# Optimization experiments

Hardware: AMD Instinct MI355X
Metric: run time of the kernel (lower is better)

The kernel has to match this reference:

```python
import jax, jax.numpy as jnp
import numpy as np

EPS = 1e-5

def conv3d(x, w):
    # x: [B,C,D,H,W], w: [O,I,3,3,3], stride 1, padding 1 (size preserving)
    return jax.lax.conv_general_dilated(
        x, w, window_strides=(1, 1, 1),
        padding=((1, 1), (1, 1), (1, 1)),
        dimension_numbers=('NCDHW', 'OIDHW', 'NCDHW'))

def deconv3d(x, w):
    # ConvTranspose3d(k=3, s=1, p=1) == conv3d with spatially flipped kernel, in/out swapped
    # torch ConvTranspose3d weight layout: [in, out, kD, kH, kW]
    wc = jnp.flip(w, axis=(2, 3, 4)).transpose(1, 0, 2, 3, 4)
    return conv3d(x, wc)

def batchnorm(x, bn):
    # bn: [4, C] rows = (gamma, beta, running_mean, running_var); inference mode
    g, b, m, v = bn[0], bn[1], bn[2], bn[3]
    scale = g * jax.lax.rsqrt(v + EPS)
    shift = b - m * scale
    return x * scale[None, :, None, None, None] + shift[None, :, None, None, None]

def qrnn_scan(Z, F, reverse):
    # gated linear recurrence h_t = f_t*h_{t-1} + (1-f_t)*z_t over depth axis (dim 2)
    Zs = jnp.moveaxis(Z, 2, 0)  # [D,B,C,H,W]
    Fs = jnp.moveaxis(F, 2, 0)
    def step(h, zf):
        z, f = zf
        h = f * h + (1.0 - f) * z
        return h, h
    h0 = jnp.zeros_like(Zs[0])  # h=None in torch == h=0 since f*0 vanishes
    _, hs = jax.lax.scan(step, h0, (Zs, Fs), reverse=reverse)
    return jnp.moveaxis(hs, 0, 2)

def qrnn_layer(x, w, bn, hidden, reverse, upsample, transpose):
    if upsample:
        # nn.Upsample(scale_factor=(1,2,2)) nearest
        x = jnp.repeat(jnp.repeat(x, 2, axis=3), 2, axis=4)
    g = deconv3d(x, w) if transpose else conv3d(x, w)
    g = batchnorm(g, bn)
    Z, F = g[:, :hidden], g[:, hidden:]
    return qrnn_scan(jnp.tanh(Z), jax.nn.sigmoid(F), reverse)

def setup_inputs():
    key = jax.random.key(0)
    ks = jax.random.split(key, 12)
    B, D = 4, 31
    x = jax.random.normal(ks[0], (B, 64, D, 32, 32), jnp.float32)
    xs2 = jax.random.normal(ks[1], (B, 32, D, 64, 64), jnp.float32)
    xs1 = jax.random.normal(ks[2], (B, 32, D, 64, 64), jnp.float32)
    xs0 = jax.random.normal(ks[3], (B, 16, D, 128, 128), jnp.float32)
    def wconv(k, shape):
        fan_in = shape[1] * 27
        return jax.random.normal(k, shape, jnp.float32) / np.float32(np.sqrt(fan_in))
    # layer0: UpsampleConv3d 64 -> 32 hidden (gates 64): Conv3d weight [64,64,3,3,3]
    w0 = wconv(ks[4], (64, 64, 3, 3, 3))
    # layer1: DeConv3D 32 -> 32 hidden (gates 64): ConvTranspose weight [in=32,out=64,3,3,3]
    w1 = wconv(ks[5], (32, 64, 3, 3, 3))
    # layer2: UpsampleConv3d 32 -> 16 hidden (gates 32): Conv3d weight [32,32,3,3,3]
    w2 = wconv(ks[6], (32, 32, 3, 3, 3))
    # layer3: DeConv3D 16 -> 16 hidden (gates 32): ConvTranspose weight [16,32,3,3,3]
    w3 = wconv(ks[7], (16, 32, 3, 3, 3))
    def mkbn(k, c):
        k1, k2, k3, k4 = jax.random.split(k, 4)
        return jnp.stack([
            jax.random.uniform(k1, (c,), jnp.float32, 0.5, 1.5),   # gamma
            jax.random.normal(k2, (c,), jnp.float32) * 0.1,        # beta
            jax.random.normal(k3, (c,), jnp.float32) * 0.1,        # running mean
            jax.random.uniform(k4, (c,), jnp.float32, 0.5, 1.5)])  # running var
    bn0 = mkbn(ks[8], 64)
    bn1 = mkbn(ks[9], 64)
    bn2 = mkbn(ks[10], 32)
    bn3 = mkbn(ks[11], 32)
    return dict(x=x, xs0=xs0, xs1=xs1, xs2=xs2,
                w0=w0, w1=w1, w2=w2, w3=w3,
                bn0=bn0, bn1=bn1, bn2=bn2, bn3=bn3)

def reference(x, xs0, xs1, xs2, w0, w1, w2, w3, bn0, bn1, bn2, bn3):
    # QRNN3DDecoder.forward with has_ad=True, reverse=False; scan direction alternates.
    # xs are popped last-first: xs2, xs1, xs0.
    h = qrnn_layer(x, w0, bn0, 32, False, True, False)          # upsample conv -> [B,32,D,64,64]
    h = qrnn_layer(h + xs2, w1, bn1, 32, True, False, True)     # deconv        -> [B,32,D,64,64]
    h = qrnn_layer(h + xs1, w2, bn2, 16, False, True, False)    # upsample conv -> [B,16,D,128,128]
    h = qrnn_layer(h + xs0, w3, bn3, 16, True, False, True)     # deconv        -> [B,16,D,128,128]
    return h
```

## Files before the change

kernel.cpp:

```cpp
#include <hip/hip_runtime.h>
#include <math.h>

#define BB 4
#define DD 31

typedef _Float16 half8 __attribute__((ext_vector_type(8)));
typedef float f32x4 __attribute__((ext_vector_type(4)));

__device__ __forceinline__ int swz(int b) { return b ^ (((b >> 7) & 7) << 4); }
__device__ __forceinline__ half8 ldswz(const _Float16* lin, int byteoff) {
    return *(const half8*)((const char*)lin + swz(byteoff));
}
__device__ __forceinline__ void stswz(_Float16* lin, int byteoff, half8 v) {
    *(half8*)((char*)lin + swz(byteoff)) = v;
}
__device__ __forceinline__ float fast_tanh(float y) {
    float e = __expf(2.f * y);
    return 1.f - 2.f * __builtin_amdgcn_rcpf(e + 1.f);
}
__device__ __forceinline__ float fast_sigmoid(float y) {
    return __builtin_amdgcn_rcpf(1.f + __expf(-y));
}


__global__ void bnprep(const float* __restrict__ bn, int C, float* __restrict__ sh) {
    int c = threadIdx.x;
    if (c >= C) return;
    float g = bn[c], b = bn[C + c], m = bn[2 * C + c], v = bn[3 * C + c];
    sh[c] = b - m * (g * rsqrtf(v + 1e-5f));
}

__global__ void wprepA(const float* __restrict__ src, const float* __restrict__ bn,
                       _Float16* __restrict__ dst, int CIN, int COUT, int KS, int tr) {
    int idx = blockIdx.x * 256 + threadIdx.x;
    int total = KS * 32 * COUT;
    if (idx >= total) return;
    int ki = idx % 32;
    int co = (idx / 32) % COUT;
    int ko = idx / (32 * COUT);
    int k = ko * 32 + ki;
    float v = 0.f;
    if (k < 27 * CIN) {
        int tap = k / CIN, ci = k % CIN;
        v = tr ? src[((size_t)ci * COUT + co) * 27 + (26 - tap)]
               : src[((size_t)co * CIN + ci) * 27 + tap];
        v *= bn[co] * rsqrtf(bn[3 * COUT + co] + 1e-5f);
    }
    dst[((size_t)ko * COUT + co) * 32 + ki] = (_Float16)v;
}

__global__ void wprepC(const float* __restrict__ src, const float* __restrict__ bn,
                       _Float16* __restrict__ dst, int CIN, int COUT, int KS, int tr) {
    int idx = blockIdx.x * 256 + threadIdx.x;
    int total = KS * 1024;
    if (idx >= total) return;
    int ki = idx & 31;
    int c16 = (idx >> 5) & 15;
    int n = (idx >> 9) & 1;
    int ko = idx >> 10;
    int co = n * (COUT / 2) + c16;
    int k = ko * 32 + ki;
    float v = 0.f;
    if (k < 27 * CIN) {
        int tap = k / CIN, ci = k % CIN;
        v = tr ? src[((size_t)ci * COUT + co) * 27 + (26 - tap)]
               : src[((size_t)co * CIN + ci) * 27 + tap];
        v *= bn[co] * rsqrtf(bn[3 * COUT + co] + 1e-5f);
    }
    dst[idx] = (_Float16)v;
}

__global__ void wprep_upA(const float* __restrict__ src, const float* __restrict__ bn,
                          _Float16* __restrict__ dst, int CIN, int COUT) {
    const int KS = 12 * CIN / 32;
    int idx = blockIdx.x * 256 + threadIdx.x;
    int total = 4 * KS * 32 * COUT;
    if (idx >= total) return;
    int ki = idx % 32;
    int co = (idx / 32) % COUT;
    int ko = (idx / (32 * COUT)) % KS;
    int par = idx / (32 * COUT * KS);
    int k = ko * 32 + ki;
    int ci = k % CIN, tap = k / CIN;
    int kd = tap >> 2, ih = (tap >> 1) & 1, iw = tap & 1;
    int ph = par >> 1, pw = par & 1;
    const float c[2][2][3] = {{{1, 0, 0}, {0, 1, 1}}, {{1, 1, 0}, {0, 0, 1}}};
    float v = 0.f;
    for (int kh = 0; kh < 3; ++kh)
        for (int kw = 0; kw < 3; ++kw)
            v += c[ph][ih][kh] * c[pw][iw][kw] *
                 src[((size_t)co * CIN + ci) * 27 + kd * 9 + kh * 3 + kw];
    v *= bn[co] * rsqrtf(bn[3 * COUT + co] + 1e-5f);
    dst[(((size_t)par * KS + ko) * COUT + co) * 32 + ki] = (_Float16)v;
}

__global__ void wprep_upB(const float* __restrict__ src, const float* __restrict__ bn,
                          _Float16* __restrict__ dst, int CIN, int COUT, int KS) {
    int idx = blockIdx.x * 256 + threadIdx.x;
    int total = 4 * KS * 1024;
    if (idx >= total) return;
    int ki = idx & 31;
    int c16 = (idx >> 5) & 15;
    int n = (idx >> 9) & 1;
    int ko = (idx >> 10) % KS;
    int par = idx / (KS * 1024);
    int co = n * (COUT / 2) + c16;
    int k = ko * 32 + ki;
    int ci = k % CIN, tap = k / CIN;
    int kd = tap >> 2, ih = (tap >> 1) & 1, iw = tap & 1;
    int ph = par >> 1, pw = par & 1;
    const float c[2][2][3] = {{{1, 0, 0}, {0, 1, 1}}, {{1, 1, 0}, {0, 0, 1}}};
    float v = 0.f;
    for (int kh = 0; kh < 3; ++kh)
        for (int kw = 0; kw < 3; ++kw)
            v += c[ph][ih][kh] * c[pw][iw][kw] *
                 src[((size_t)co * CIN + ci) * 27 + kd * 9 + kh * 3 + kw];
    v *= bn[co] * rsqrtf(bn[3 * COUT + co] + 1e-5f);
    dst[idx] = (_Float16)v;
}

__global__ __launch_bounds__(256) void xconv(const float* __restrict__ src,
                                             _Float16* __restrict__ dst) {
    int idx = blockIdx.x * 256 + threadIdx.x;
    if (idx >= 4 * 31 * 1024 * 8) return;
    int cb = idx & 7;
    int pos = (idx >> 3) & 1023;
    int bd = idx >> 13;
    int d = bd % 31, b = bd / 31;
    half8 v;
#pragma unroll
    for (int j = 0; j < 8; ++j)
        v[j] = (_Float16)src[(((size_t)b * 64 + cb * 8 + j) * 31 + d) * 1024 + pos];
    *(half8*)(dst + ((size_t)bd * 1024 + pos) * 64 + cb * 8) = v;
}

__global__ __launch_bounds__(256) void xst_pb(const float* __restrict__ src,
                                              _Float16* __restrict__ dst) {
    int hw = blockIdx.x * 256 + threadIdx.x;
    int bd = blockIdx.y;
    int d = bd % DD, b = bd / DD;
    int h = hw >> 7, w = hw & 127;
    int par = (h & 1) * 2 + (w & 1);
    int p = (h >> 1) * 64 + (w >> 1);
    _Float16 tmp[16];
#pragma unroll
    for (int c = 0; c < 16; ++c)
        tmp[c] = (_Float16)src[((size_t)(b * 16 + c) * DD + d) * 16384 + hw];
    _Float16* o = dst + (((size_t)bd * 4 + par) * 4096 + p) * 16;
    *(half8*)o = *(half8*)tmp;
    *(half8*)(o + 8) = *(half8*)(tmp + 8);
}

template <int CIN, int COUT, int S, int MINW>
__global__ __launch_bounds__(256, MINW) void conv_up(
    const _Float16* __restrict__ inp, const _Float16* __restrict__ wqu,
    const float* __restrict__ bnsh, _Float16* __restrict__ gout) {
    constexpr int SIN = S / 2;
    constexpr int KS = 12 * CIN / 32;
    constexpr int NCB = COUT / 16;
    constexpr int NC8 = CIN / 8;
    constexpr int IH = 6, IW = 18;
    constexpr int PATCH = 3 * IH * IW;

    __shared__ __align__(16) _Float16 lin[PATCH * CIN];

    const int tid = threadIdx.x;
    const int lane = tid & 63;
    const int wv = tid >> 6;
    const int col = lane & 15;
    const int grp = lane >> 4;
    const int ph = wv >> 1, pw = wv & 1;

    const int bwp = blockIdx.x * 16;
    const int bhp = blockIdx.y * 4;
    const int bz = blockIdx.z;
    const int d = bz % DD;

    for (int idx = tid; idx < PATCH * NC8; idx += 256) {
        int c8 = idx % NC8;
        int pos = idx / NC8;
        int iwp = pos % IW, t = pos / IW;
        int ihp = t % IH, kd = t / IH;
        int dz = d + kd - 1, gh = bhp - 1 + ihp, gw = bwp - 1 + iwp;
        half8 v = {0, 0, 0, 0, 0, 0, 0, 0};
        if ((unsigned)dz < (unsigned)DD && (unsigned)gh < (unsigned)SIN &&
            (unsigned)gw < (unsigned)SIN)
            v = *(const half8*)(inp +
                (((size_t)(bz + kd - 1) * SIN + gh) * SIN + gw) * CIN + c8 * 8);
        *(half8*)((char*)lin + swz((pos * CIN + c8 * 8) * 2)) = v;
    }
    __syncthreads();

    f32x4 acc[4][NCB];
#pragma unroll
    for (int f = 0; f < 4; ++f)
#pragma unroll
        for (int n = 0; n < NCB; ++n) acc[f][n] = {0.f, 0.f, 0.f, 0.f};

    const _Float16* wqp = wqu + (size_t)(ph * 2 + pw) * KS * COUT * 32;

#pragma unroll
    for (int ko = 0; ko < KS; ++ko) {
        int tap = (ko * 32) / CIN;
        int ci = (ko * 32) % CIN + grp * 8;
        int kd = tap >> 2, ih = (tap >> 1) & 1, iwk = tap & 1;

        int lcol = col + iwk + pw;
        int r0 = ih + ph;
        int cb = ((kd * IH + r0) * IW + lcol) * CIN + ci;
        half8 a[4];
#pragma unroll
        for (int f = 0; f < 4; ++f)
            a[f] = ldswz(lin, (cb + f * IW * CIN) * 2);

        half8 bfr[NCB];
#pragma unroll
        for (int n = 0; n < NCB; ++n)
            bfr[n] = *(const half8*)(wqp + ((ko * COUT + n * 16 + col) * 32 + grp * 8));
#pragma unroll
        for (int f = 0; f < 4; ++f)
#pragma unroll
            for (int n = 0; n < NCB; ++n)
                acc[f][n] = __builtin_amdgcn_mfma_f32_16x16x32_f16(a[f], bfr[n],
                                                                   acc[f][n], 0, 0, 0);
    }

    const size_t obase = (size_t)bz * S * S * COUT;
#pragma unroll
    for (int n = 0; n < NCB; ++n) {
        int co = n * 16 + col;
        float sh = bnsh[co];
#pragma unroll
        for (int f = 0; f < 4; ++f) {
            int h = 2 * (bhp + f) + ph;
#pragma unroll
            for (int r = 0; r < 4; ++r) {
                int w = 2 * (bwp + grp * 4 + r) + pw;
                float y = acc[f][n][r] + sh;
                float v = (n < NCB / 2) ? fast_tanh(y) : fast_sigmoid(y);
                gout[obase + ((size_t)h * S + w) * COUT + co] = (_Float16)v;
            }
        }
    }
}

template <int CIN, int COUT, int S, int KSTEPS>
__global__ __launch_bounds__(256, 2) void conv_mfma(
    const _Float16* __restrict__ inp, const _Float16* __restrict__ wq,
    const float* __restrict__ bnsh, _Float16* __restrict__ gout) {
    constexpr int IH = 18;
    constexpr int IW = 18;
    constexpr int NCB = COUT / 16;
    constexpr int NC8 = CIN / 8;
    constexpr int PATCH = 3 * IH * IW;

    __shared__ __align__(16) _Float16 lin[PATCH * CIN];

    const int tid = threadIdx.x;
    const int lane = tid & 63;
    const int wv = tid >> 6;
    const int col = lane & 15;
    const int grp = lane >> 4;

    const int w0 = blockIdx.x * 16;
    const int h0 = blockIdx.y * 16;
    const int bz = blockIdx.z;
    const int d = bz % DD;

    const int ibh = h0 - 1;
    const int ibw = w0 - 1;

    for (int idx = tid; idx < PATCH * NC8; idx += 256) {
        int c8 = idx % NC8;
        int pos = idx / NC8;
        int iw = pos % IW, t = pos / IW;
        int ih = t % IH, kd = t / IH;
        int dz = d + kd - 1, gh = ibh + ih, gw = ibw + iw;
        half8 v = {0, 0, 0, 0, 0, 0, 0, 0};
        if ((unsigned)dz < (unsigned)DD && (unsigned)gh < (unsigned)S &&
            (unsigned)gw < (unsigned)S)
            v = *(const half8*)(inp +
                (((size_t)(bz + kd - 1) * S + gh) * S + gw) * CIN + c8 * 8);
        *(half8*)((char*)lin + swz((pos * CIN + c8 * 8) * 2)) = v;
    }
    __syncthreads();

    f32x4 acc[4][NCB];
#pragma unroll
    for (int f = 0; f < 4; ++f)
#pragma unroll
        for (int n = 0; n < NCB; ++n) acc[f][n] = {0.f, 0.f, 0.f, 0.f};

#pragma unroll
    for (int ko = 0; ko < KSTEPS; ++ko) {
        int tap = (ko * 32) / CIN;
        int kd = tap / 9, kh = (tap / 3) % 3, kw = tap % 3;
        int ci = (ko * 32) % CIN + grp * 8;

        half8 a[4];
        int iw = col + kw;
        int cb = ((kd * IH + wv * 4 + kh) * IW + iw) * CIN + ci;
#pragma unroll
        for (int f = 0; f < 4; ++f)
            a[f] = ldswz(lin, (cb + f * IW * CIN) * 2);

        half8 bfr[NCB];
#pragma unroll
        for (int n = 0; n < NCB; ++n)
            bfr[n] = *(const half8*)(wq + ((ko * COUT + n * 16 + col) * 32 + grp * 8));
#pragma unroll
        for (int f = 0; f < 4; ++f)
#pragma unroll
            for (int n = 0; n < NCB; ++n)
                acc[f][n] = __builtin_amdgcn_mfma_f32_16x16x32_f16(a[f], bfr[n],
                                                                   acc[f][n], 0, 0, 0);
    }

    const size_t obase = (size_t)bz * S * S * COUT;
#pragma unroll
    for (int n = 0; n < NCB; ++n) {
        int co = n * 16 + col;
        float sh = bnsh[co];
#pragma unroll
        for (int f = 0; f < 4; ++f) {
            int h = h0 + wv * 4 + f;
#pragma unroll
            for (int r = 0; r < 4; ++r) {
                int w = w0 + grp * 4 + r;
                float y = acc[f][n][r] + sh;
                float v = (n < NCB / 2) ? fast_tanh(y) : fast_sigmoid(y);
                gout[obase + ((size_t)h * S + w) * COUT + co] = (_Float16)v;
            }
        }
    }
}

template <int H, int HW>
__global__ __launch_bounds__(256) void qscan(
    const _Float16* __restrict__ g, const float* __restrict__ xs,
    _Float16* __restrict__ hout, int rev) {
    constexpr int NCB = H / 8;
    int idx = blockIdx.x * 256 + threadIdx.x;
    if (idx >= BB * HW * NCB) return;
    int cb = idx % NCB;
    int hw = (idx / NCB) % HW;
    int b = idx / (NCB * HW);
    int c0 = cb * 8;

    float h[8];
#pragma unroll
    for (int j = 0; j < 8; ++j) h[j] = 0.f;

    for (int t = 0; t < DD; ++t) {
        int d = rev ? (DD - 1 - t) : t;
        const _Float16* gp = g + ((size_t)(b * DD + d) * HW + hw) * (2 * H);
        half8 z8 = *(const half8*)(gp + c0);
        half8 f8 = *(const half8*)(gp + H + c0);
        half8 o;
#pragma unroll
        for (int j = 0; j < 8; ++j) {
            float fv = (float)f8[j];
            h[j] = fv * h[j] + (1.f - fv) * (float)z8[j];
            o[j] = (_Float16)(h[j] + xs[(((size_t)b * H + c0 + j) * DD + d) * HW + hw]);
        }
        *(half8*)(hout + ((size_t)(b * DD + d) * HW + hw) * H + c0) = o;
    }
}

template <int CIN, int S, int HID, int KS, int REV>
__global__ __launch_bounds__(256, 2) void fconv_up1(
    const _Float16* __restrict__ inp,
    const _Float16* __restrict__ wq,
    const float* __restrict__ bnsh,
    const _Float16* __restrict__ xs,
    _Float16* __restrict__ hout) {

    constexpr int SIN = S / 2;
    constexpr int IW = 18;
    constexpr int IHP = 6;
    constexpr int NC8 = CIN / 8;
    constexpr int P8 = IHP * IW * NC8;
    constexpr int NST = (P8 + 255) / 256;
    constexpr int PLANEB = IHP * IW * CIN * 2;
    constexpr int LWB = 3 * PLANEB;
    constexpr int WH = KS * 1024;

    __shared__ __align__(16) _Float16 lds[(LWB / 2) + WH];

    const int tid = threadIdx.x;
    const int lane = tid & 63;
    const int wv = tid >> 6;
    const int col = lane & 15;
    const int grp = lane >> 4;

    const int bwp = blockIdx.x * 16;
    const int bhp = blockIdx.y * 4;
    const int par = blockIdx.z & 3;
    const int b = blockIdx.z >> 2;
    const size_t bbase = (size_t)b * DD;

    const float shz = bnsh[col];
    const float shf = bnsh[HID + col];
    const int hc = col;
    const _Float16* wqb = wq + (size_t)par * KS * 1024;

    auto stage_now = [&](int dz) {
        int slot = (dz + 33) % 3;
        for (int idx = tid; idx < P8; idx += 256) {
            int c8 = idx % NC8;
            int pos = idx / NC8;
            int ih = pos / IW, iw = pos % IW;
            int gh = bhp - 1 + ih, gw = bwp - 1 + iw;
            half8 v = {0, 0, 0, 0, 0, 0, 0, 0};
            if ((unsigned)dz < (unsigned)DD && (unsigned)gh < (unsigned)SIN &&
                (unsigned)gw < (unsigned)SIN)
                v = *(const half8*)(inp + (((bbase + dz) * SIN + gh) * SIN + gw) * CIN + c8 * 8);
            stswz(lds, slot * PLANEB + (pos * CIN + c8 * 8) * 2, v);
        }
    };

    constexpr int dir = REV ? -1 : 1;
    const int d0 = REV ? DD - 1 : 0;
    stage_now(d0 - dir);
    stage_now(d0);
    stage_now(d0 + dir);
    for (int i = tid; i < WH / 8; i += 256) {
        half8 v = *(const half8*)(wqb + i * 8);
        stswz(lds, LWB + i * 16, v);
    }
    __syncthreads();

    float hst[4];
#pragma unroll
    for (int r = 0; r < 4; ++r) hst[r] = 0.f;

    const int ph = par >> 1, pw = par & 1;
    (void)ph; (void)pw;

    for (int t = 0; t < DD; ++t) {
        const int d = d0 + dir * t;
        const int dzl = d + 2 * dir;
        const int sm = (d - 1 + 33) % 3;
        const int s0 = (d + 33) % 3;
        const int sp = (d + 1 + 33) % 3;
        const int scommit = REV ? sp : sm;

        half8 sv[NST];
#pragma unroll
        for (int i = 0; i < NST; ++i) {
            int idx = tid + i * 256;
            half8 v = {0, 0, 0, 0, 0, 0, 0, 0};
            if (idx < P8) {
                int c8 = idx % NC8;
                int pos = idx / NC8;
                int ih = pos / IW, iw = pos % IW;
                int gh = bhp - 1 + ih, gw = bwp - 1 + iw;
                if ((unsigned)dzl < (unsigned)DD && (unsigned)gh < (unsigned)SIN &&
                    (unsigned)gw < (unsigned)SIN)
                    v = *(const half8*)(inp +
                        (((bbase + dzl) * SIN + gh) * SIN + gw) * CIN + c8 * 8);
            }
            sv[i] = v;
        }

        f32x4 accz = {0.f, 0.f, 0.f, 0.f};
        f32x4 accf = {0.f, 0.f, 0.f, 0.f};
#pragma unroll
        for (int ko = 0; ko < KS; ++ko) {
            int tap = (ko * 32) / CIN;
            int ci = (ko * 32) % CIN + grp * 8;
            int kd = tap >> 2, ihh = (tap >> 1) & 1, iwk = tap & 1;
            int slot = kd == 0 ? sm : (kd == 1 ? s0 : sp);
            int lcol = col + iwk + pw;
            int row = wv + ihh + ph;
            half8 a = ldswz(lds, slot * PLANEB + ((row * IW + lcol) * CIN + ci) * 2);
            half8 bf0 = ldswz(lds, LWB + (ko * 1024 + col * 32 + grp * 8) * 2);
            half8 bf1 = ldswz(lds, LWB + (ko * 1024 + 512 + col * 32 + grp * 8) * 2);
            accz = __builtin_amdgcn_mfma_f32_16x16x32_f16(a, bf0, accz, 0, 0, 0);
            accf = __builtin_amdgcn_mfma_f32_16x16x32_f16(a, bf1, accf, 0, 0, 0);
        }

        __syncthreads();
#pragma unroll
        for (int i = 0; i < NST; ++i) {
            int idx = tid + i * 256;
            if (idx < P8) {
                int c8 = idx % NC8;
                int pos = idx / NC8;
                stswz(lds, scommit * PLANEB + (pos * CIN + c8 * 8) * 2, sv[i]);
            }
        }

        const size_t pb = ((bbase + d) * 4 + par) * (size_t)(SIN * SIN);
        const int hp = bhp + wv;
#pragma unroll
        for (int r = 0; r < 4; ++r) {
            int wp = bwp + grp * 4 + r;
            size_t sp2 = pb + hp * SIN + wp;
            float z = fast_tanh(accz[r] + shz);
            float fg = fast_sigmoid(accf[r] + shf);
            hst[r] = fg * hst[r] + (1.f - fg) * z;
            float xv = (float)xs[sp2 * HID + hc];
            hout[sp2 * HID + hc] = (_Float16)(hst[r] + xv);
        }
        __syncthreads();
    }
}

template <int CIN, int S, int HID, int KS, int NF, int REV>
__global__ __launch_bounds__(256, 2) void fconv3(
    const _Float16* __restrict__ inp,
    const _Float16* __restrict__ wq,
    const float* __restrict__ bnsh,
    float* __restrict__ fout) {

    constexpr int IW = 18;
    constexpr int TH = 4 * NF;
    constexpr int IHP = TH + 2;
    constexpr int NC8 = CIN / 8;
    constexpr int P8 = IHP * IW * NC8;
    constexpr int NST = (P8 + 255) / 256;
    constexpr int PLANEB = IHP * IW * CIN * 2;
    constexpr int LWB = 3 * PLANEB;
    constexpr int WH = KS * 1024;
    constexpr int SIN = S / 2;

    __shared__ __align__(16) _Float16 lds[(LWB / 2) + WH];

    const int tid = threadIdx.x;
    const int lane = tid & 63;
    const int wv = tid >> 6;
    const int col = lane & 15;
    const int grp = lane >> 4;

    const int w0 = blockIdx.x * 16;
    const int h0 = blockIdx.y * TH;
    const int b = blockIdx.z;
    const size_t bbase = (size_t)b * DD;

    const float shz = bnsh[col];
    const float shf = bnsh[HID + col];
    const int hc = col;

    auto gaddr = [&](int dz, int gh, int gw) -> size_t {
        return ((((bbase + dz) * 2 + (gh & 1)) * 2 + (gw & 1)) * (size_t)(SIN * SIN) +
                (gh >> 1) * SIN + (gw >> 1)) * CIN;
    };

    auto stage_now = [&](int dz) {
        int slot = (dz + 33) % 3;
        for (int idx = tid; idx < P8; idx += 256) {
            int c8 = idx % NC8;
            int pos = idx / NC8;
            int ih = pos / IW, iw = pos % IW;
            int gh = h0 - 1 + ih, gw = w0 - 1 + iw;
            half8 v = {0, 0, 0, 0, 0, 0, 0, 0};
            if ((unsigned)dz < (unsigned)DD && (unsigned)gh < (unsigned)S &&
                (unsigned)gw < (unsigned)S)
                v = *(const half8*)(inp + gaddr(dz, gh, gw) + c8 * 8);
            stswz(lds, slot * PLANEB + (pos * CIN + c8 * 8) * 2, v);
        }
    };

    constexpr int dir = REV ? -1 : 1;
    const int d0 = REV ? DD - 1 : 0;
    stage_now(d0 - dir);
    stage_now(d0);
    stage_now(d0 + dir);
    for (int i = tid; i < WH / 8; i += 256) {
        half8 v = *(const half8*)(wq + i * 8);
        stswz(lds, LWB + i * 16, v);
    }
    __syncthreads();

    float hst[NF][4];
#pragma unroll
    for (int f = 0; f < NF; ++f)
#pragma unroll
        for (int r = 0; r < 4; ++r) hst[f][r] = 0.f;

    for (int t = 0; t < DD; ++t) {
        const int d = d0 + dir * t;
        const int dzl = d + 2 * dir;
        const int sm = (d - 1 + 33) % 3;
        const int s0 = (d + 33) % 3;
        const int sp = (d + 1 + 33) % 3;
        const int scommit = REV ? sp : sm;

        half8 sv[NST];
#pragma unroll
        for (int i = 0; i < NST; ++i) {
            int idx = tid + i * 256;
            half8 v = {0, 0, 0, 0, 0, 0, 0, 0};
            if (idx < P8) {
                int c8 = idx % NC8;
                int pos = idx / NC8;
                int ih = pos / IW, iw = pos % IW;
                int gh = h0 - 1 + ih, gw = w0 - 1 + iw;
                if ((unsigned)dzl < (unsigned)DD && (unsigned)gh < (unsigned)S &&
                    (unsigned)gw < (unsigned)S)
                    v = *(const half8*)(inp + gaddr(dzl, gh, gw) + c8 * 8);
            }
            sv[i] = v;
        }

        f32x4 acc[NF][2];
#pragma unroll
        for (int f = 0; f < NF; ++f) {
            acc[f][0] = {0.f, 0.f, 0.f, 0.f};
            acc[f][1] = {0.f, 0.f, 0.f, 0.f};
        }
#pragma unroll
        for (int ko = 0; ko < KS; ++ko) {
            int kd, kh, kw, ci;
            if (CIN >= 32) {
                int tap = (ko * 32) / CIN;
                kd = tap / 9; kh = (tap / 3) % 3; kw = tap % 3;
                ci = (ko * 32) % CIN + grp * 8;
            } else {
                int t0 = (2 * ko < 27) ? 2 * ko : 26;
                int t1 = (2 * ko + 1 < 27) ? 2 * ko + 1 : 26;
                int hi = grp >> 1;
                kd = hi ? t1 / 9 : t0 / 9;
                kh = hi ? (t1 / 3) % 3 : (t0 / 3) % 3;
                kw = hi ? t1 % 3 : t0 % 3;
                ci = (grp & 1) * 8;
            }
            int slot = kd == 0 ? sm : (kd == 1 ? s0 : sp);
            int iw = col + kw;
            half8 a[NF];
#pragma unroll
            for (int f = 0; f < NF; ++f)
                a[f] = ldswz(lds, slot * PLANEB +
                             (((wv * NF + f + kh) * IW + iw) * CIN + ci) * 2);
            half8 bf0 = ldswz(lds, LWB + (ko * 1024 + col * 32 + grp * 8) * 2);
            half8 bf1 = ldswz(lds, LWB + (ko * 1024 + 512 + col * 32 + grp * 8) * 2);
#pragma unroll
            for (int f = 0; f < NF; ++f) {
                acc[f][0] = __builtin_amdgcn_mfma_f32_16x16x32_f16(a[f], bf0, acc[f][0], 0, 0, 0);
                acc[f][1] = __builtin_amdgcn_mfma_f32_16x16x32_f16(a[f], bf1, acc[f][1], 0, 0, 0);
            }
        }

        __syncthreads();
#pragma unroll
        for (int i = 0; i < NST; ++i) {
            int idx = tid + i * 256;
            if (idx < P8) {
                int c8 = idx % NC8;
                int pos = idx / NC8;
                stswz(lds, scommit * PLANEB + (pos * CIN + c8 * 8) * 2, sv[i]);
            }
        }

#pragma unroll
        for (int f = 0; f < NF; ++f) {
            int h = h0 + wv * NF + f;
#pragma unroll
            for (int r = 0; r < 4; ++r) {
                int w = w0 + grp * 4 + r;
                size_t sp2 = (size_t)h * S + w;
                float z = fast_tanh(acc[f][0][r] + shz);
                float fg = fast_sigmoid(acc[f][1][r] + shf);
                hst[f][r] = fg * hst[f][r] + (1.f - fg) * z;
                fout[(((size_t)b * HID + hc) * DD + d) * ((size_t)S * S) + sp2] = hst[f][r];
            }
        }
        __syncthreads();
    }
}

extern "C" void kernel_launch(void* const* d_in, const int* in_sizes, int n_in,
                              void* d_out, int out_size, void* d_ws, size_t ws_size,
                              hipStream_t stream) {
    const float* x   = (const float*)d_in[0];
    const float* xs0 = (const float*)d_in[1];
    const float* xs1 = (const float*)d_in[2];
    const float* xs2 = (const float*)d_in[3];
    const float* w0  = (const float*)d_in[4];
    const float* w1  = (const float*)d_in[5];
    const float* w2  = (const float*)d_in[6];
    const float* w3  = (const float*)d_in[7];
    const float* bn0 = (const float*)d_in[8];
    const float* bn1 = (const float*)d_in[9];
    const float* bn2 = (const float*)d_in[10];
    const float* bn3 = (const float*)d_in[11];
    float* out = (float*)d_out;

    char* p = (char*)d_ws;
    _Float16* xf   = (_Float16*)p; p += (size_t)124 * 1024 * 64 * 2;
    _Float16* gA   = (_Float16*)p; p += (size_t)124 * 4096 * 64 * 2;
    _Float16* hA   = (_Float16*)p; p += (size_t)124 * 4096 * 32 * 2;
    _Float16* hA2  = (_Float16*)p; p += (size_t)124 * 4096 * 32 * 2;
    _Float16* hB   = (_Float16*)p; p += (size_t)124 * 16384 * 16 * 2;
    _Float16* xs0f = (_Float16*)p; p += (size_t)124 * 16384 * 16 * 2;
    _Float16* wq0u = (_Float16*)p; p += (size_t)4 * 24 * 64 * 32 * 2;
    _Float16* wq1  = (_Float16*)p; p += (size_t)27 * 64 * 32 * 2;
    _Float16* wq2u = (_Float16*)p; p += (size_t)4 * 12 * 1024 * 2;
    _Float16* wq3  = (_Float16*)p; p += (size_t)14 * 1024 * 2;
    float* sh0 = (float*)p; p += 64 * 4;
    float* sh1 = (float*)p; p += 64 * 4;
    float* sh2 = (float*)p; p += 64 * 4;
    float* sh3 = (float*)p; p += 64 * 4;

    xconv<<<(4 * 31 * 1024 * 8 + 255) / 256, 256, 0, stream>>>(x, xf);
    xst_pb<<<dim3(64, BB * DD), 256, 0, stream>>>(xs0, xs0f);
    wprep_upA<<<(4 * 24 * 32 * 64 + 255) / 256, 256, 0, stream>>>(w0, bn0, wq0u, 64, 64);
    wprepA<<<(27 * 32 * 64 + 255) / 256, 256, 0, stream>>>(w1, bn1, wq1, 32, 64, 27, 1);
    wprep_upB<<<(4 * 12 * 1024 + 255) / 256, 256, 0, stream>>>(w2, bn2, wq2u, 32, 32, 12);
    wprepC<<<(14 * 1024 + 255) / 256, 256, 0, stream>>>(w3, bn3, wq3, 16, 32, 14, 1);
    bnprep<<<1, 64, 0, stream>>>(bn0, 64, sh0);
    bnprep<<<1, 64, 0, stream>>>(bn1, 64, sh1);
    bnprep<<<1, 64, 0, stream>>>(bn2, 32, sh2);
    bnprep<<<1, 64, 0, stream>>>(bn3, 32, sh3);

    conv_up<64, 64, 64, 3><<<dim3(2, 8, BB * DD), 256, 0, stream>>>(xf, wq0u, sh0, gA);
    qscan<32, 4096><<<(BB * 4096 * 4 + 255) / 256, 256, 0, stream>>>(gA, xs2, hA, 0);

    conv_mfma<32, 64, 64, 27><<<dim3(4, 4, BB * DD), 256, 0, stream>>>(hA, wq1, sh1, gA);
    qscan<32, 4096><<<(BB * 4096 * 4 + 255) / 256, 256, 0, stream>>>(gA, xs1, hA2, 1);

    fconv_up1<32, 128, 16, 12, 0><<<dim3(4, 16, BB * 4), 256, 0, stream>>>(
        hA2, wq2u, sh2, xs0f, hB);

    fconv3<16, 128, 16, 14, 2, 1><<<dim3(8, 16, BB), 256, 0, stream>>>(
        hB, wq3, sh3, out);
}
```

Measured before the change: 510.0 us.

## Stage conv epilogue outputs through LDS and pre-transpose skip inputs to fp16 channel-last

The conv_up and conv_mfma epilogues now write activated gate values into swizzled shared memory and then emit coalesced 16-byte vector stores per pixel, replacing scattered 2-byte global stores. The xs2 and xs1 skip tensors are converted up front by a new transpose kernel into fp16 channel-last layout, so qscan reads one half8 per step instead of eight strided fp32 loads. The fused later kernels also get a higher minimum-occupancy launch bound. The cost is two extra conversion passes and extra workspace, plus possible register pressure or spills from the tighter launch bounds.

```diff
diff --git a/kernel.cpp b/kernel.cpp
--- a/kernel.cpp
+++ b/kernel.cpp
@@ -134,6 +134,21 @@
     *(half8*)(dst + ((size_t)bd * 1024 + pos) * 64 + cb * 8) = v;
 }
 
+template <int C, int HW>
+__global__ __launch_bounds__(256) void xst(const float* __restrict__ src,
+                                           _Float16* __restrict__ dst) {
+    int hw = blockIdx.x * 256 + threadIdx.x;
+    int bd = blockIdx.y;
+    int d = bd % DD, b = bd / DD;
+    _Float16 tmp[C];
+#pragma unroll
+    for (int c = 0; c < C; ++c)
+        tmp[c] = (_Float16)src[((size_t)(b * C + c) * DD + d) * HW + hw];
+#pragma unroll
+    for (int c8 = 0; c8 < C / 8; ++c8)
+        *(half8*)(dst + ((size_t)bd * HW + hw) * C + c8 * 8) = *(half8*)(tmp + c8 * 8);
+}
+
 __global__ __launch_bounds__(256) void xst_pb(const float* __restrict__ src,
                                               _Float16* __restrict__ dst) {
     int hw = blockIdx.x * 256 + threadIdx.x;
@@ -225,22 +240,33 @@
                                                                    acc[f][n], 0, 0, 0);
     }
 
-    const size_t obase = (size_t)bz * S * S * COUT;
+    __syncthreads();
 #pragma unroll
     for (int n = 0; n < NCB; ++n) {
         int co = n * 16 + col;
         float sh = bnsh[co];
 #pragma unroll
         for (int f = 0; f < 4; ++f) {
-            int h = 2 * (bhp + f) + ph;
+            int lh = 2 * f + ph;
 #pragma unroll
             for (int r = 0; r < 4; ++r) {
-                int w = 2 * (bwp + grp * 4 + r) + pw;
+                int lw = 2 * (grp * 4 + r) + pw;
                 float y = acc[f][n][r] + sh;
                 float v = (n < NCB / 2) ? fast_tanh(y) : fast_sigmoid(y);
-                gout[obase + ((size_t)h * S + w) * COUT + co] = (_Float16)v;
-            }
-        }
+                *(_Float16*)((char*)lin + swz(((lh * 32 + lw) * COUT + co) * 2)) =
+                    (_Float16)v;
+            }
+        }
+    }
+    __syncthreads();
+    {
+        int lh = tid >> 5, lw = tid & 31;
+        _Float16* gp = gout + (size_t)bz * S * S * COUT +
+                       ((size_t)(2 * bhp + lh) * S + (2 * bwp + lw)) * COUT;
+        int base = (lh * 32 + lw) * COUT * 2;
+#pragma unroll
+        for (int i = 0; i < COUT / 8; ++i)
+            *(half8*)(gp + i * 8) = ldswz(lin, base + i * 16);
     }
 }
 
@@ -316,28 +342,39 @@
                                                                    acc[f][n], 0, 0, 0);
     }
 
-    const size_t obase = (size_t)bz * S * S * COUT;
+    __syncthreads();
 #pragma unroll
     for (int n = 0; n < NCB; ++n) {
         int co = n * 16 + col;
         float sh = bnsh[co];
 #pragma unroll
         for (int f = 0; f < 4; ++f) {
-            int h = h0 + wv * 4 + f;
+            int lh = wv * 4 + f;
 #pragma unroll
             for (int r = 0; r < 4; ++r) {
-                int w = w0 + grp * 4 + r;
+                int lw = grp * 4 + r;
                 float y = acc[f][n][r] + sh;
                 float v = (n < NCB / 2) ? fast_tanh(y) : fast_sigmoid(y);
-                gout[obase + ((size_t)h * S + w) * COUT + co] = (_Float16)v;
-            }
-        }
+                *(_Float16*)((char*)lin + swz(((lh * 16 + lw) * COUT + co) * 2)) =
+                    (_Float16)v;
+            }
+        }
+    }
+    __syncthreads();
+    {
+        int lh = tid >> 4, lw = tid & 15;
+        _Float16* gp = gout + (size_t)bz * S * S * COUT +
+                       ((size_t)(h0 + lh) * S + (w0 + lw)) * COUT;
+        int base = (lh * 16 + lw) * COUT * 2;
+#pragma unroll
+        for (int i = 0; i < COUT / 8; ++i)
+            *(half8*)(gp + i * 8) = ldswz(lin, base + i * 16);
     }
 }
 
 template <int H, int HW>
 __global__ __launch_bounds__(256) void qscan(
-    const _Float16* __restrict__ g, const float* __restrict__ xs,
+    const _Float16* __restrict__ g, const _Float16* __restrict__ xs,
     _Float16* __restrict__ hout, int rev) {
     constexpr int NCB = H / 8;
     int idx = blockIdx.x * 256 + threadIdx.x;
@@ -353,22 +390,24 @@
 
     for (int t = 0; t < DD; ++t) {
         int d = rev ? (DD - 1 - t) : t;
-        const _Float16* gp = g + ((size_t)(b * DD + d) * HW + hw) * (2 * H);
+        size_t pix = (size_t)(b * DD + d) * HW + hw;
+        const _Float16* gp = g + pix * (2 * H);
         half8 z8 = *(const half8*)(gp + c0);
         half8 f8 = *(const half8*)(gp + H + c0);
+        half8 x8 = *(const half8*)(xs + pix * H + c0);
         half8 o;
 #pragma unroll
         for (int j = 0; j < 8; ++j) {
             float fv = (float)f8[j];
             h[j] = fv * h[j] + (1.f - fv) * (float)z8[j];
-            o[j] = (_Float16)(h[j] + xs[(((size_t)b * H + c0 + j) * DD + d) * HW + hw]);
-        }
-        *(half8*)(hout + ((size_t)(b * DD + d) * HW + hw) * H + c0) = o;
+            o[j] = (_Float16)(h[j] + (float)x8[j]);
+        }
+        *(half8*)(hout + pix * H + c0) = o;
     }
 }
 
 template <int CIN, int S, int HID, int KS, int REV>
-__global__ __launch_bounds__(256, 2) void fconv_up1(
+__global__ __launch_bounds__(256, 3) void fconv_up1(
     const _Float16* __restrict__ inp,
     const _Float16* __restrict__ wq,
     const float* __restrict__ bnsh,
@@ -435,7 +474,6 @@
     for (int r = 0; r < 4; ++r) hst[r] = 0.f;
 
     const int ph = par >> 1, pw = par & 1;
-    (void)ph; (void)pw;
 
     for (int t = 0; t < DD; ++t) {
         const int d = d0 + dir * t;
@@ -508,7 +546,7 @@
 }
 
 template <int CIN, int S, int HID, int KS, int NF, int REV>
-__global__ __launch_bounds__(256, 2) void fconv3(
+__global__ __launch_bounds__(256, 3) void fconv3(
     const _Float16* __restrict__ inp,
     const _Float16* __restrict__ wq,
     const float* __restrict__ bnsh,
@@ -694,6 +732,8 @@
     _Float16* hA2  = (_Float16*)p; p += (size_t)124 * 4096 * 32 * 2;
     _Float16* hB   = (_Float16*)p; p += (size_t)124 * 16384 * 16 * 2;
     _Float16* xs0f = (_Float16*)p; p += (size_t)124 * 16384 * 16 * 2;
+    _Float16* xs2f = (_Float16*)p; p += (size_t)124 * 4096 * 32 * 2;
+    _Float16* xs1f = (_Float16*)p; p += (size_t)124 * 4096 * 32 * 2;
     _Float16* wq0u = (_Float16*)p; p += (size_t)4 * 24 * 64 * 32 * 2;
     _Float16* wq1  = (_Float16*)p; p += (size_t)27 * 64 * 32 * 2;
     _Float16* wq2u = (_Float16*)p; p += (size_t)4 * 12 * 1024 * 2;
@@ -705,6 +745,8 @@
 
     xconv<<<(4 * 31 * 1024 * 8 + 255) / 256, 256, 0, stream>>>(x, xf);
     xst_pb<<<dim3(64, BB * DD), 256, 0, stream>>>(xs0, xs0f);
+    xst<32, 4096><<<dim3(16, BB * DD), 256, 0, stream>>>(xs2, xs2f);
+    xst<32, 4096><<<dim3(16, BB * DD), 256, 0, stream>>>(xs1, xs1f);
     wprep_upA<<<(4 * 24 * 32 * 64 + 255) / 256, 256, 0, stream>>>(w0, bn0, wq0u, 64, 64);
     wprepA<<<(27 * 32 * 64 + 255) / 256, 256, 0, stream>>>(w1, bn1, wq1, 32, 64, 27, 1);
     wprep_upB<<<(4 * 12 * 1024 + 255) / 256, 256, 0, stream>>>(w2, bn2, wq2u, 32, 32, 12);
@@ -715,10 +757,10 @@
     bnprep<<<1, 64, 0, stream>>>(bn3, 32, sh3);
 
     conv_up<64, 64, 64, 3><<<dim3(2, 8, BB * DD), 256, 0, stream>>>(xf, wq0u, sh0, gA);
-    qscan<32, 4096><<<(BB * 4096 * 4 + 255) / 256, 256, 0, stream>>>(gA, xs2, hA, 0);
+    qscan<32, 4096><<<(BB * 4096 * 4 + 255) / 256, 256, 0, stream>>>(gA, xs2f, hA, 0);
 
     conv_mfma<32, 64, 64, 27><<<dim3(4, 4, BB * DD), 256, 0, stream>>>(hA, wq1, sh1, gA);
-    qscan<32, 4096><<<(BB * 4096 * 4 + 255) / 256, 256, 0, stream>>>(gA, xs1, hA2, 1);
+    qscan<32, 4096><<<(BB * 4096 * 4 + 255) / 256, 256, 0, stream>>>(gA, xs1f, hA2, 1);
 
     fconv_up1<32, 128, 16, 12, 0><<<dim3(4, 16, BB * 4), 256, 0, stream>>>(
         hA2, wq2u, sh2, xs0f, hB);
```

New measurement: 580.3 us. 13.8% more time.
